# Kernel optimization log

Measured on AMD Instinct MI355X. Metric: run time of the kernel, lower is better.

The kernel has to match this reference:

```python
import jax, jax.numpy as jnp
import numpy as np

B, t, FEAT, N, E = 128, 16, 256, 1024, 8192


def setup_inputs() -> dict:
    key = jax.random.key(0)
    k = jax.random.split(key, 9)
    s = 1.0 / np.sqrt(FEAT).astype(np.float32)
    x = jax.random.normal(k[0], (B, t, FEAT), jnp.float32)
    nodes = jax.random.normal(k[1], (B, N, FEAT), jnp.float32)
    edges = jax.random.randint(k[2], (B, 2, E), 0, 256).astype(jnp.int32)
    weights = jax.random.uniform(k[3], (B, 1, E), jnp.float32)
    T = jax.random.randint(k[4], (B,), 0, N - t).astype(jnp.int32)
    taus = jnp.full((B,), t, dtype=jnp.int32)  # no ragged padding: taus == t
    W_self1 = jax.random.normal(k[5], (FEAT, FEAT), jnp.float32) * s
    W_msg1 = jax.random.normal(k[6], (FEAT, FEAT), jnp.float32) * s
    W_self2 = jax.random.normal(k[7], (FEAT, FEAT), jnp.float32) * s
    W_msg2 = jax.random.normal(k[8], (FEAT, FEAT), jnp.float32) * s
    return dict(x=x, taus=taus, nodes=nodes, edges=edges, weights=weights, T=T,
                W_self1=W_self1, W_msg1=W_msg1, W_self2=W_self2, W_msg2=W_msg2)


def _gcm(x, nodes, weights, edges, T, Ws1, Wm1, Ws2, Wm2):
    Bn, tn, feat = x.shape
    Nn = nodes.shape[1]
    # --- scatter new nodes into the fixed-size node buffer ---
    b_idx = jnp.repeat(jnp.arange(Bn), tn)                       # [B*t]
    tau_idx = (T[:, None] + jnp.arange(tn)).reshape(-1)          # [B*t]
    nodes = nodes.at[b_idx, tau_idx].set(x.reshape(Bn * tn, feat))
    # --- to_batch: flatten ragged per-batch graphs into one big graph ---
    flat = nodes.reshape(Bn * Nn, feat)                          # [B*N, feat]
    off = (jnp.arange(Bn) * Nn)[:, None]                         # per-batch node offset
    valid = (edges[:, 0] >= 0) & (edges[:, 1] >= 0)              # -1 marks invalid edges
    src = jnp.where(valid, edges[:, 0] + off, 0).reshape(-1)     # [B*E]
    dst = jnp.where(valid, edges[:, 1] + off, 0).reshape(-1)
    ew = (weights[:, 0] * valid).reshape(-1)                     # invalid edges -> weight 0
    # --- 2-layer edge-weighted GraphConv GNN (tanh activation) ---
    def layer(h, Ws, Wm):
        agg = jax.ops.segment_sum(ew[:, None] * h[src], dst, num_segments=Bn * Nn)
        return jnp.tanh(h @ Ws + agg @ Wm)
    h = layer(flat, Ws1, Wm1)
    h = layer(h, Ws2, Wm2)
    # --- gather GNN outputs for the newly inserted nodes ---
    out_idx = b_idx * Nn + tau_idx
    mx = h[out_idx].reshape(Bn, tn, feat)
    return mx, nodes


def reference(x, taus, nodes, edges, weights, T, W_self1, W_msg1, W_self2, W_msg2):
    mx, new_nodes = _gcm(x, nodes, weights, edges, T, W_self1, W_msg1, W_self2, W_msg2)
    return (mx, new_nodes, edges, weights, T + taus)
```

## Files before the change

kernel.cpp:

```cpp
#include <hip/hip_runtime.h>
#include <math.h>

#define BB    128
#define TTW   16
#define FEATN 256
#define NNODE 1024
#define NEDGE 8192
#define MROW  272
#define M1    (BB*MROW)

#define OUT_MX    0
#define OUT_NODES (BB*TTW*FEATN)
#define OUT_EDGES (OUT_NODES + BB*NNODE*FEATN)
#define OUT_W     (OUT_EDGES + BB*2*NEDGE)
#define OUT_TT    (OUT_W + BB*NEDGE)

#define R_PASS_END  8388608
#define R_WIN_END   (R_PASS_END + 131072)
#define R_EDG_END   (R_WIN_END + 524288)
#define R_W_END     (R_EDG_END + 262144)
#define R_WC_END    (R_W_END + 262144)
#define R_TT_END    (R_WC_END + 128)
#define PREP_BLOCKS (BB + (R_TT_END + 255) / 256)

typedef short bf16x8 __attribute__((ext_vector_type(8)));
typedef float f32x4  __attribute__((ext_vector_type(4)));

__device__ inline unsigned short f2bf(float f) {
    unsigned int u = __float_as_uint(f);
    return (unsigned short)((u + 0x7fffu + ((u >> 16) & 1u)) >> 16);
}
__device__ inline float tanh_fast(float x) {
    return 1.f - 2.f / (__expf(2.f * x) + 1.f);
}

__global__ void k_prep(const float* __restrict__ x, const int* __restrict__ taus,
                       const float* __restrict__ nodes, const int* __restrict__ edges,
                       const float* __restrict__ weights, const int* __restrict__ T,
                       const float* __restrict__ Ws1, const float* __restrict__ Wm1,
                       const float* __restrict__ Ws2, const float* __restrict__ Wm2,
                       float* __restrict__ out, unsigned short* __restrict__ Xc1,
                       unsigned short* __restrict__ Wt1, unsigned short* __restrict__ Wt2,
                       int2* __restrict__ sw, int* __restrict__ bstart) {
    __shared__ int cnt[256];
    __shared__ int pos[256];
    if (blockIdx.x < BB) {
        int b = blockIdx.x, tid = threadIdx.x;
        cnt[tid] = 0;
        __syncthreads();
        const int* src = edges + (size_t)b * 2 * NEDGE;
        const int* dst = src + NEDGE;
        for (int e = tid; e < NEDGE; e += 256) atomicAdd(&cnt[dst[e]], 1);
        __syncthreads();
        int my = cnt[tid], v = my;
        for (int off = 1; off < 256; off <<= 1) {
            int u = 0;
            if (tid >= off) u = cnt[tid - off];
            __syncthreads();
            cnt[tid] = v = v + u;
            __syncthreads();
        }
        int start = v - my;
        bstart[b * 264 + tid] = start;
        if (tid == 0) bstart[b * 264 + 256] = NEDGE;
        pos[tid] = start;
        __syncthreads();
        const float* wb = weights + (size_t)b * NEDGE;
        for (int e = tid; e < NEDGE; e += 256) {
            int d = dst[e];
            int p = atomicAdd(&pos[d], 1);
            sw[(size_t)b * NEDGE + p] = make_int2(src[e], __float_as_int(wb[e]));
        }
        return;
    }

    int idx = (blockIdx.x - BB) * 256 + threadIdx.x;
    if (idx < R_PASS_END) {
        int b = idx >> 16, row = (idx >> 6) & 1023, f = idx & 63;
        int dT = row - T[b];
        const float4* src = ((unsigned)dT < 16u)
                                ? ((const float4*)x + ((size_t)b * 16 + dT) * 64 + f)
                                : ((const float4*)nodes + idx);
        float4 v = *src;
        ((float4*)(out + OUT_NODES))[idx] = v;
        if (row < 256) {
            uint2 p;
            p.x = f2bf(v.x) | ((unsigned)f2bf(v.y) << 16);
            p.y = f2bf(v.z) | ((unsigned)f2bf(v.w) << 16);
            *(uint2*)(Xc1 + ((size_t)(b * MROW + row)) * 512 + f * 4) = p;
        }
    } else if (idx < R_WIN_END) {
        int j = idx - R_PASS_END;
        int b = j >> 10, i = (j >> 6) & 15, f = j & 63;
        float4 v = ((const float4*)x)[((size_t)b * 16 + i) * 64 + f];
        uint2 p;
        p.x = f2bf(v.x) | ((unsigned)f2bf(v.y) << 16);
        p.y = f2bf(v.z) | ((unsigned)f2bf(v.w) << 16);
        *(uint2*)(Xc1 + ((size_t)(b * MROW + 256 + i)) * 512 + f * 4) = p;
    } else if (idx < R_EDG_END) {
        int j = idx - R_WIN_END;
        int4 e = ((const int4*)edges)[j];
        ((float4*)(out + OUT_EDGES))[j] =
            make_float4((float)e.x, (float)e.y, (float)e.z, (float)e.w);
    } else if (idx < R_W_END) {
        int j = idx - R_EDG_END;
        ((float4*)(out + OUT_W))[j] = ((const float4*)weights)[j];
    } else if (idx < R_WC_END) {
        int j = idx - R_W_END;
        int layer = j >> 17, q = j & 131071;
        int k = q >> 8, n = q & 255;
        const float* Ws = layer ? Ws2 : Ws1;
        const float* Wm = layer ? Wm2 : Wm1;
        float v = (k < 256) ? Ws[(size_t)k * 256 + n] : Wm[(size_t)(k - 256) * 256 + n];
        (layer ? Wt2 : Wt1)[(size_t)n * 512 + k] = f2bf(v);
    } else if (idx < R_TT_END) {
        int b = idx - R_WC_END;
        out[OUT_TT + b] = (float)(T[b] + taus[b]);
    }
}

__global__ void k_spmm1(const int2* __restrict__ sw, const int* __restrict__ bstart,
                        const int* __restrict__ T, unsigned short* __restrict__ Xc1) {
    int g    = blockIdx.x * 4 + (threadIdx.x >> 6);
    int lane = threadIdx.x & 63;
    int b = g / MROW;
    int r = g - b * MROW;
    int d = (r < 256) ? r : (T[b] + r - 256);
    float4 acc = make_float4(0.f, 0.f, 0.f, 0.f);
    if (d < 256) {
        int e0 = bstart[b * 264 + d];
        int e1 = bstart[b * 264 + d + 1];
        const int2* swb = sw + (size_t)b * NEDGE;
        const unsigned short* xb = Xc1 + (size_t)b * MROW * 512;
        for (int e = e0; e < e1; ++e) {
            int2 p = swb[e];
            float wt = __int_as_float(p.y);
            uint2 q = *((const uint2*)(xb + (size_t)p.x * 512) + lane);
            acc.x = fmaf(wt, __uint_as_float(q.x << 16),          acc.x);
            acc.y = fmaf(wt, __uint_as_float(q.x & 0xffff0000u),  acc.y);
            acc.z = fmaf(wt, __uint_as_float(q.y << 16),          acc.z);
            acc.w = fmaf(wt, __uint_as_float(q.y & 0xffff0000u),  acc.w);
        }
    }
    uint2 o;
    o.x = f2bf(acc.x) | ((unsigned)f2bf(acc.y) << 16);
    o.y = f2bf(acc.z) | ((unsigned)f2bf(acc.w) << 16);
    *(uint2*)(Xc1 + (size_t)g * 512 + 256 + lane * 4) = o;
}

template <int OBF16>
__global__ __launch_bounds__(256, 2) void k_gemm(const unsigned short* __restrict__ Xc,
                                                 const unsigned short* __restrict__ Wt,
                                                 void* __restrict__ outp) {
    int tile_m = blockIdx.x >> 1;
    int tile_n = blockIdx.x & 1;
    int tid  = threadIdx.x;
    int wv   = tid >> 6, lane = tid & 63;
    int wm   = wv >> 1, wn = wv & 1;
    int lm   = lane & 15, lq = lane >> 4;

    __shared__ short As[128 * 32];
    __shared__ short Bs[128 * 32];

    f32x4 acc[4][4];
#pragma unroll
    for (int mi = 0; mi < 4; ++mi)
#pragma unroll
        for (int ni = 0; ni < 4; ++ni) acc[mi][ni] = (f32x4){0.f, 0.f, 0.f, 0.f};

    for (int kc = 0; kc < 16; ++kc) {
        if (kc) __syncthreads();
#pragma unroll
        for (int p = 0; p < 2; ++p) {
            int slot = p * 256 + tid;
            int row = slot >> 2, seg = slot & 3;
            ((uint4*)As)[slot] = *(const uint4*)(Xc + ((size_t)(tile_m * 128 + row)) * 512 + kc * 32 + seg * 8);
            ((uint4*)Bs)[slot] = *(const uint4*)(Wt + ((size_t)(tile_n * 128 + row)) * 512 + kc * 32 + seg * 8);
        }
        __syncthreads();

        bf16x8 af[4], bfr[4];
#pragma unroll
        for (int mi = 0; mi < 4; ++mi)
            af[mi] = ((const bf16x8*)As)[(wm * 64 + mi * 16 + lm) * 4 + lq];
#pragma unroll
        for (int ni = 0; ni < 4; ++ni)
            bfr[ni] = ((const bf16x8*)Bs)[(wn * 64 + ni * 16 + lm) * 4 + lq];
#pragma unroll
        for (int mi = 0; mi < 4; ++mi)
#pragma unroll
            for (int ni = 0; ni < 4; ++ni)
                acc[mi][ni] = __builtin_amdgcn_mfma_f32_16x16x32_bf16(af[mi], bfr[ni], acc[mi][ni], 0, 0, 0);
    }

#pragma unroll
    for (int mi = 0; mi < 4; ++mi) {
#pragma unroll
        for (int ni = 0; ni < 4; ++ni) {
            int n = tile_n * 128 + wn * 64 + ni * 16 + lm;
#pragma unroll
            for (int r = 0; r < 4; ++r) {
                int m = tile_m * 128 + wm * 64 + mi * 16 + lq * 4 + r;
                float v = tanh_fast(acc[mi][ni][r]);
                if (OBF16) ((unsigned short*)outp)[(size_t)m * 256 + n] = f2bf(v);
                else       ((float*)outp)[(size_t)m * 256 + n] = v;
            }
        }
    }
}

__global__ void k_agg2(const unsigned short* __restrict__ h1, const int2* __restrict__ sw,
                       const int* __restrict__ bstart, const int* __restrict__ T,
                       unsigned short* __restrict__ Xc2) {
    int g2   = blockIdx.x * 4 + (threadIdx.x >> 6);
    int lane = threadIdx.x & 63;
    int b = g2 >> 4, i = g2 & 15;
    ((uint2*)(Xc2 + (size_t)g2 * 512))[lane] =
        ((const uint2*)(h1 + (size_t)(b * MROW + 256 + i) * 256))[lane];
    int d = T[b] + i;
    float4 acc = make_float4(0.f, 0.f, 0.f, 0.f);
    if (d < 256) {
        int e0 = bstart[b * 264 + d];
        int e1 = bstart[b * 264 + d + 1];
        const int2* swb = sw + (size_t)b * NEDGE;
        const unsigned short* hb = h1 + (size_t)b * MROW * 256;
        for (int e = e0; e < e1; ++e) {
            int2 p = swb[e];
            float wt = __int_as_float(p.y);
            uint2 q = *((const uint2*)(hb + (size_t)p.x * 256) + lane);
            acc.x = fmaf(wt, __uint_as_float(q.x << 16),          acc.x);
            acc.y = fmaf(wt, __uint_as_float(q.x & 0xffff0000u),  acc.y);
            acc.z = fmaf(wt, __uint_as_float(q.y << 16),          acc.z);
            acc.w = fmaf(wt, __uint_as_float(q.y & 0xffff0000u),  acc.w);
        }
    }
    uint2 o;
    o.x = f2bf(acc.x) | ((unsigned)f2bf(acc.y) << 16);
    o.y = f2bf(acc.z) | ((unsigned)f2bf(acc.w) << 16);
    *(uint2*)(Xc2 + (size_t)g2 * 512 + 256 + lane * 4) = o;
}

extern "C" void kernel_launch(void* const* d_in, const int* in_sizes, int n_in,
                              void* d_out, int out_size, void* d_ws, size_t ws_size,
                              hipStream_t stream) {
    const float* x       = (const float*)d_in[0];
    const int*   taus    = (const int*)d_in[1];
    const float* nodes   = (const float*)d_in[2];
    const int*   edges   = (const int*)d_in[3];
    const float* weights = (const float*)d_in[4];
    const int*   T       = (const int*)d_in[5];
    const float* Ws1     = (const float*)d_in[6];
    const float* Wm1     = (const float*)d_in[7];
    const float* Ws2     = (const float*)d_in[8];
    const float* Wm2     = (const float*)d_in[9];
    float* out = (float*)d_out;

    char* ws = (char*)d_ws;
    int2*           sw     = (int2*)ws;
    int*            bstart = (int*)(ws + 8388608);
    unsigned short* Xc1    = (unsigned short*)(ws + 8523776);
    unsigned short* h1     = (unsigned short*)(ws + 44175360);
    unsigned short* Xc2    = (unsigned short*)(ws + 62001152);
    unsigned short* Wt1    = (unsigned short*)(ws + 64098304);
    unsigned short* Wt2    = (unsigned short*)(ws + 64360448);

    k_prep  <<<PREP_BLOCKS, 256, 0, stream>>>(x, taus, nodes, edges, weights, T,
                                              Ws1, Wm1, Ws2, Wm2,
                                              out, Xc1, Wt1, Wt2, sw, bstart);
    k_spmm1 <<<M1 / 4, 256, 0, stream>>>(sw, bstart, T, Xc1);
    k_gemm<1><<<272 * 2, 256, 0, stream>>>(Xc1, Wt1, h1);
    k_agg2  <<<512, 256, 0, stream>>>(h1, sw, bstart, T, Xc2);
    k_gemm<0><<<16 * 2, 256, 0, stream>>>(Xc2, Wt2, out + OUT_MX);
}
```

Before: 450.0 us.

## Use nontemporal copies, direct-to-LDS GEMM loads, batched edge gathers, XCD-aware block mapping

Bulk copies in the prep kernel now use nontemporal loads and stores, so streaming data does not pollute the cache. The GEMM stages tiles with global_load_lds straight into shared memory instead of going through registers. The SpMM and aggregation kernels load 64 edge entries per wave at once, broadcast them with readlane, and unroll the feature gathers by four to raise memory-level parallelism. Block indices are remapped so that consecutive blocks across the eight XCDs cover the same batch rows, which should improve L2 locality. The inner unroll steps by four edges without masking the tail, so when an edge count is not a multiple of four it reads beyond the valid range; those lanes return (0,0) from the padded loads only if the lane index stays below 64.

```diff
diff --git a/kernel.cpp b/kernel.cpp
--- a/kernel.cpp
+++ b/kernel.cpp
@@ -32,6 +32,10 @@
 }
 __device__ inline float tanh_fast(float x) {
     return 1.f - 2.f / (__expf(2.f * x) + 1.f);
+}
+__device__ inline void gl_lds16(const unsigned short* g, short* l) {
+    __builtin_amdgcn_global_load_lds((const __attribute__((address_space(1))) void*)g,
+                                     (__attribute__((address_space(3))) void*)l, 16, 0, 0);
 }
 
 __global__ void k_prep(const float* __restrict__ x, const int* __restrict__ taus,
@@ -78,11 +82,10 @@
     if (idx < R_PASS_END) {
         int b = idx >> 16, row = (idx >> 6) & 1023, f = idx & 63;
         int dT = row - T[b];
-        const float4* src = ((unsigned)dT < 16u)
-                                ? ((const float4*)x + ((size_t)b * 16 + dT) * 64 + f)
-                                : ((const float4*)nodes + idx);
-        float4 v = *src;
-        ((float4*)(out + OUT_NODES))[idx] = v;
+        f32x4 v;
+        if ((unsigned)dT < 16u) v = ((const f32x4*)x)[((size_t)b * 16 + dT) * 64 + f];
+        else                    v = __builtin_nontemporal_load((const f32x4*)nodes + idx);
+        __builtin_nontemporal_store(v, (f32x4*)(out + OUT_NODES) + idx);
         if (row < 256) {
             uint2 p;
             p.x = f2bf(v.x) | ((unsigned)f2bf(v.y) << 16);
@@ -92,7 +95,7 @@
     } else if (idx < R_WIN_END) {
         int j = idx - R_PASS_END;
         int b = j >> 10, i = (j >> 6) & 15, f = j & 63;
-        float4 v = ((const float4*)x)[((size_t)b * 16 + i) * 64 + f];
+        f32x4 v = ((const f32x4*)x)[((size_t)b * 16 + i) * 64 + f];
         uint2 p;
         p.x = f2bf(v.x) | ((unsigned)f2bf(v.y) << 16);
         p.y = f2bf(v.z) | ((unsigned)f2bf(v.w) << 16);
@@ -100,11 +103,13 @@
     } else if (idx < R_EDG_END) {
         int j = idx - R_WIN_END;
         int4 e = ((const int4*)edges)[j];
-        ((float4*)(out + OUT_EDGES))[j] =
-            make_float4((float)e.x, (float)e.y, (float)e.z, (float)e.w);
+        f32x4 o;
+        o.x = (float)e.x; o.y = (float)e.y; o.z = (float)e.z; o.w = (float)e.w;
+        __builtin_nontemporal_store(o, (f32x4*)(out + OUT_EDGES) + j);
     } else if (idx < R_W_END) {
         int j = idx - R_EDG_END;
-        ((float4*)(out + OUT_W))[j] = ((const float4*)weights)[j];
+        f32x4 v = __builtin_nontemporal_load((const f32x4*)weights + j);
+        __builtin_nontemporal_store(v, (f32x4*)(out + OUT_W) + j);
     } else if (idx < R_WC_END) {
         int j = idx - R_W_END;
         int layer = j >> 17, q = j & 131071;
@@ -121,10 +126,12 @@
 
 __global__ void k_spmm1(const int2* __restrict__ sw, const int* __restrict__ bstart,
                         const int* __restrict__ T, unsigned short* __restrict__ Xc1) {
-    int g    = blockIdx.x * 4 + (threadIdx.x >> 6);
+    int p = blockIdx.x;
+    int inner = p >> 3;
+    int b = (inner / 68) * 8 + (p & 7);
+    int r = (inner % 68) * 4 + (threadIdx.x >> 6);
     int lane = threadIdx.x & 63;
-    int b = g / MROW;
-    int r = g - b * MROW;
+    int g = b * MROW + r;
     int d = (r < 256) ? r : (T[b] + r - 256);
     float4 acc = make_float4(0.f, 0.f, 0.f, 0.f);
     if (d < 256) {
@@ -132,14 +139,41 @@
         int e1 = bstart[b * 264 + d + 1];
         const int2* swb = sw + (size_t)b * NEDGE;
         const unsigned short* xb = Xc1 + (size_t)b * MROW * 512;
-        for (int e = e0; e < e1; ++e) {
-            int2 p = swb[e];
-            float wt = __int_as_float(p.y);
-            uint2 q = *((const uint2*)(xb + (size_t)p.x * 512) + lane);
-            acc.x = fmaf(wt, __uint_as_float(q.x << 16),          acc.x);
-            acc.y = fmaf(wt, __uint_as_float(q.x & 0xffff0000u),  acc.y);
-            acc.z = fmaf(wt, __uint_as_float(q.y << 16),          acc.z);
-            acc.w = fmaf(wt, __uint_as_float(q.y & 0xffff0000u),  acc.w);
+        for (int ce = e0; ce < e1; ce += 64) {
+            int2 pl = (ce + lane < e1) ? swb[ce + lane] : make_int2(0, 0);
+            int cnt = e1 - ce; if (cnt > 64) cnt = 64;
+            for (int i = 0; i < cnt; i += 4) {
+                int x0 = __builtin_amdgcn_readlane(pl.x, i + 0);
+                int y0 = __builtin_amdgcn_readlane(pl.y, i + 0);
+                int x1 = __builtin_amdgcn_readlane(pl.x, i + 1);
+                int y1 = __builtin_amdgcn_readlane(pl.y, i + 1);
+                int x2 = __builtin_amdgcn_readlane(pl.x, i + 2);
+                int y2 = __builtin_amdgcn_readlane(pl.y, i + 2);
+                int x3 = __builtin_amdgcn_readlane(pl.x, i + 3);
+                int y3 = __builtin_amdgcn_readlane(pl.y, i + 3);
+                uint2 q0 = *((const uint2*)(xb + (size_t)x0 * 512) + lane);
+                uint2 q1 = *((const uint2*)(xb + (size_t)x1 * 512) + lane);
+                uint2 q2 = *((const uint2*)(xb + (size_t)x2 * 512) + lane);
+                uint2 q3 = *((const uint2*)(xb + (size_t)x3 * 512) + lane);
+                float w0 = __int_as_float(y0), w1 = __int_as_float(y1);
+                float w2 = __int_as_float(y2), w3 = __int_as_float(y3);
+                acc.x = fmaf(w0, __uint_as_float(q0.x << 16),         acc.x);
+                acc.y = fmaf(w0, __uint_as_float(q0.x & 0xffff0000u), acc.y);
+                acc.z = fmaf(w0, __uint_as_float(q0.y << 16),         acc.z);
+                acc.w = fmaf(w0, __uint_as_float(q0.y & 0xffff0000u), acc.w);
+                acc.x = fmaf(w1, __uint_as_float(q1.x << 16),         acc.x);
+                acc.y = fmaf(w1, __uint_as_float(q1.x & 0xffff0000u), acc.y);
+                acc.z = fmaf(w1, __uint_as_float(q1.y << 16),         acc.z);
+                acc.w = fmaf(w1, __uint_as_float(q1.y & 0xffff0000u), acc.w);
+                acc.x = fmaf(w2, __uint_as_float(q2.x << 16),         acc.x);
+                acc.y = fmaf(w2, __uint_as_float(q2.x & 0xffff0000u), acc.y);
+                acc.z = fmaf(w2, __uint_as_float(q2.y << 16),         acc.z);
+                acc.w = fmaf(w2, __uint_as_float(q2.y & 0xffff0000u), acc.w);
+                acc.x = fmaf(w3, __uint_as_float(q3.x << 16),         acc.x);
+                acc.y = fmaf(w3, __uint_as_float(q3.x & 0xffff0000u), acc.y);
+                acc.z = fmaf(w3, __uint_as_float(q3.y << 16),         acc.z);
+                acc.w = fmaf(w3, __uint_as_float(q3.y & 0xffff0000u), acc.w);
+            }
         }
     }
     uint2 o;
@@ -168,15 +202,17 @@
 #pragma unroll
         for (int ni = 0; ni < 4; ++ni) acc[mi][ni] = (f32x4){0.f, 0.f, 0.f, 0.f};
 
+    const unsigned short* Ag = Xc + (size_t)(tile_m * 128 + wv * 32 + (lane >> 2)) * 512 + (lane & 3) * 8;
+    const unsigned short* Bg = Wt + (size_t)(tile_n * 128 + wv * 32 + (lane >> 2)) * 512 + (lane & 3) * 8;
+    short* Al = As + (wv * 2) * 512 + lane * 8;
+    short* Bl = Bs + (wv * 2) * 512 + lane * 8;
+
     for (int kc = 0; kc < 16; ++kc) {
         if (kc) __syncthreads();
-#pragma unroll
-        for (int p = 0; p < 2; ++p) {
-            int slot = p * 256 + tid;
-            int row = slot >> 2, seg = slot & 3;
-            ((uint4*)As)[slot] = *(const uint4*)(Xc + ((size_t)(tile_m * 128 + row)) * 512 + kc * 32 + seg * 8);
-            ((uint4*)Bs)[slot] = *(const uint4*)(Wt + ((size_t)(tile_n * 128 + row)) * 512 + kc * 32 + seg * 8);
-        }
+        gl_lds16(Ag + kc * 32,              Al);
+        gl_lds16(Ag + kc * 32 + 16 * 512,   Al + 512);
+        gl_lds16(Bg + kc * 32,              Bl);
+        gl_lds16(Bg + kc * 32 + 16 * 512,   Bl + 512);
         __syncthreads();
 
         bf16x8 af[4], bfr[4];
@@ -212,9 +248,12 @@
 __global__ void k_agg2(const unsigned short* __restrict__ h1, const int2* __restrict__ sw,
                        const int* __restrict__ bstart, const int* __restrict__ T,
                        unsigned short* __restrict__ Xc2) {
-    int g2   = blockIdx.x * 4 + (threadIdx.x >> 6);
+    int p = blockIdx.x;
+    int inner = p >> 3;
+    int b = (inner / 4) * 8 + (p & 7);
+    int i = (inner % 4) * 4 + (threadIdx.x >> 6);
     int lane = threadIdx.x & 63;
-    int b = g2 >> 4, i = g2 & 15;
+    int g2 = b * 16 + i;
     ((uint2*)(Xc2 + (size_t)g2 * 512))[lane] =
         ((const uint2*)(h1 + (size_t)(b * MROW + 256 + i) * 256))[lane];
     int d = T[b] + i;
@@ -224,14 +263,41 @@
         int e1 = bstart[b * 264 + d + 1];
         const int2* swb = sw + (size_t)b * NEDGE;
         const unsigned short* hb = h1 + (size_t)b * MROW * 256;
-        for (int e = e0; e < e1; ++e) {
-            int2 p = swb[e];
-            float wt = __int_as_float(p.y);
-            uint2 q = *((const uint2*)(hb + (size_t)p.x * 256) + lane);
-            acc.x = fmaf(wt, __uint_as_float(q.x << 16),          acc.x);
-            acc.y = fmaf(wt, __uint_as_float(q.x & 0xffff0000u),  acc.y);
-            acc.z = fmaf(wt, __uint_as_float(q.y << 16),          acc.z);
-            acc.w = fmaf(wt, __uint_as_float(q.y & 0xffff0000u),  acc.w);
+        for (int ce = e0; ce < e1; ce += 64) {
+            int2 pl = (ce + lane < e1) ? swb[ce + lane] : make_int2(0, 0);
+            int cnt = e1 - ce; if (cnt > 64) cnt = 64;
+            for (int ii = 0; ii < cnt; ii += 4) {
+                int x0 = __builtin_amdgcn_readlane(pl.x, ii + 0);
+                int y0 = __builtin_amdgcn_readlane(pl.y, ii + 0);
+                int x1 = __builtin_amdgcn_readlane(pl.x, ii + 1);
+                int y1 = __builtin_amdgcn_readlane(pl.y, ii + 1);
+                int x2 = __builtin_amdgcn_readlane(pl.x, ii + 2);
+                int y2 = __builtin_amdgcn_readlane(pl.y, ii + 2);
+                int x3 = __builtin_amdgcn_readlane(pl.x, ii + 3);
+                int y3 = __builtin_amdgcn_readlane(pl.y, ii + 3);
+                uint2 q0 = *((const uint2*)(hb + (size_t)x0 * 256) + lane);
+                uint2 q1 = *((const uint2*)(hb + (size_t)x1 * 256) + lane);
+                uint2 q2 = *((const uint2*)(hb + (size_t)x2 * 256) + lane);
+                uint2 q3 = *((const uint2*)(hb + (size_t)x3 * 256) + lane);
+                float w0 = __int_as_float(y0), w1 = __int_as_float(y1);
+                float w2 = __int_as_float(y2), w3 = __int_as_float(y3);
+                acc.x = fmaf(w0, __uint_as_float(q0.x << 16),         acc.x);
+                acc.y = fmaf(w0, __uint_as_float(q0.x & 0xffff0000u), acc.y);
+                acc.z = fmaf(w0, __uint_as_float(q0.y << 16),         acc.z);
+                acc.w = fmaf(w0, __uint_as_float(q0.y & 0xffff0000u), acc.w);
+                acc.x = fmaf(w1, __uint_as_float(q1.x << 16),         acc.x);
+                acc.y = fmaf(w1, __uint_as_float(q1.x & 0xffff0000u), acc.y);
+                acc.z = fmaf(w1, __uint_as_float(q1.y << 16),         acc.z);
+                acc.w = fmaf(w1, __uint_as_float(q1.y & 0xffff0000u), acc.w);
+                acc.x = fmaf(w2, __uint_as_float(q2.x << 16),         acc.x);
+                acc.y = fmaf(w2, __uint_as_float(q2.x & 0xffff0000u), acc.y);
+                acc.z = fmaf(w2, __uint_as_float(q2.y << 16),         acc.z);
+                acc.w = fmaf(w2, __uint_as_float(q2.y & 0xffff0000u), acc.w);
+                acc.x = fmaf(w3, __uint_as_float(q3.x << 16),         acc.x);
+                acc.y = fmaf(w3, __uint_as_float(q3.x & 0xffff0000u), acc.y);
+                acc.z = fmaf(w3, __uint_as_float(q3.y << 16),         acc.z);
+                acc.w = fmaf(w3, __uint_as_float(q3.y & 0xffff0000u), acc.w);
+            }
         }
     }
     uint2 o;
```

After: 377.1 us. 16.2% less time.
